# Performance work log

Measured on AMD Instinct MI355X. Metric: run time of the kernel, lower is better.

Reference implementation:

```python
import jax, jax.numpy as jnp
import numpy as np

N = 100000      # nodes
E = 1600000     # edges (avg degree 16)
F = 128         # feature dim (in == out)
H = 4           # heads
ALPHA = 0.2     # leaky relu slope


def setup_inputs() -> dict:
    key = jax.random.key(0)
    k1, k2, k3, k4, k5 = jax.random.split(key, 5)
    inputs = jax.random.normal(k1, (N, F), dtype=jnp.float32)
    # ensure every node appears as a destination row (src of message) so rowsum > 0
    src = jnp.concatenate([jnp.arange(N, dtype=jnp.int32),
                           jax.random.randint(k2, (E - N,), 0, N, dtype=jnp.int32)])
    dst = jax.random.randint(k3, (E,), 0, N, dtype=jnp.int32)
    edge = jnp.stack([src, dst])  # [2, E], rows = adj.indices()
    adj_values = jax.random.uniform(k4, (E,), dtype=jnp.float32)
    W = jnp.ones((H, F), dtype=jnp.float32)  # nn.init.ones_ per head
    stdv = 1.0 / np.sqrt(2.0 * F)
    a = jax.random.uniform(k5, (H, 2 * F), dtype=jnp.float32, minval=-stdv, maxval=stdv)
    return {"inputs": inputs, "edge": edge, "adj_values": adj_values, "W": W, "a": a}


def reference(inputs, edge, adj_values, W, a):
    src, dst = edge[0], edge[1]
    acc = jnp.zeros_like(inputs)
    for k in range(H):  # small fixed head loop (distinct params per head)
        h = inputs * W[k]                       # [N, F] elementwise scale
        # a.mm([h_src; h_dst]) decomposes into per-node partial scores
        s_src = h @ a[k, :F]                    # [N]
        s_dst = h @ a[k, F:]                    # [N]
        e = jnp.exp(jax.nn.leaky_relu(s_src[src] + s_dst[dst], ALPHA)) * adj_values  # [E]
        rowsum = jax.ops.segment_sum(e, src, num_segments=N)               # [N]
        h_prime = jax.ops.segment_sum(e[:, None] * h[dst], src, num_segments=N)  # [N, F]
        acc = acc + jax.nn.elu(h_prime / rowsum[:, None])  # concat=True -> elu
    return acc / H  # mean over heads
```

## Files before the change

kernel.cpp:

```cpp
#include <hip/hip_runtime.h>

#define FDIM   128
#define HEADS  4
#define ALPHA  0.2f
#define DMASK  0x03FFFFFF
#define PT     4096
#define NBMAX  1568

typedef float v2f __attribute__((ext_vector_type(2)));
typedef __attribute__((ext_vector_type(8))) short bf16x8;
typedef __attribute__((ext_vector_type(4))) float f32x4;
typedef __attribute__((ext_vector_type(4))) unsigned u32x4;

__global__ __launch_bounds__(256) void score_kernel(
    const float* __restrict__ x, const float* __restrict__ W,
    const float* __restrict__ a, float* __restrict__ s_src,
    float* __restrict__ s_dst, unsigned int* __restrict__ xb,
    const int* __restrict__ src, int* __restrict__ hist,
    int E, int HB, int n) {
  __shared__ int h[NBMAX];
  int lane = threadIdx.x & 63;
  int node = (blockIdx.x << 2) + (threadIdx.x >> 6);
  if (node < n) {
    const float2* x2 = (const float2*)x;
    const float2* W2 = (const float2*)W;
    const float2* a2 = (const float2*)a;
    float2 xv = x2[(size_t)node * 64 + lane];

    unsigned int u0 = __float_as_uint(xv.x);
    unsigned int u1 = __float_as_uint(xv.y);
    u0 += 0x7fffu + ((u0 >> 16) & 1u);
    u1 += 0x7fffu + ((u1 >> 16) & 1u);
    xb[(size_t)node * 64 + lane] = (u0 >> 16) | (u1 & 0xffff0000u);

    float p[8];
#pragma unroll
    for (int k = 0; k < HEADS; k++) {
      float2 wv = W2[k * 64 + lane];
      float hx = xv.x * wv.x, hy = xv.y * wv.y;
      float2 as_ = a2[k * 128 + lane];
      float2 ad_ = a2[k * 128 + 64 + lane];
      p[k]     = hx * as_.x + hy * as_.y;
      p[4 + k] = hx * ad_.x + hy * ad_.y;
    }

    bool h5 = (lane & 32) != 0;
    float q[4];
#pragma unroll
    for (int k = 0; k < 4; k++) {
      float send = h5 ? p[k] : p[4 + k];
      float got = __shfl_xor(send, 32);
      q[k] = (h5 ? p[4 + k] : p[k]) + got;
    }
    bool h4 = (lane & 16) != 0;
    float r[2];
#pragma unroll
    for (int j = 0; j < 2; j++) {
      float send = h4 ? q[j] : q[2 + j];
      float got = __shfl_xor(send, 16);
      r[j] = (h4 ? q[2 + j] : q[j]) + got;
    }
    bool h3 = (lane & 8) != 0;
    float send = h3 ? r[0] : r[1];
    float got = __shfl_xor(send, 8);
    float v = (h3 ? r[1] : r[0]) + got;
    v += __shfl_xor(v, 1);
    v += __shfl_xor(v, 2);
    v += __shfl_xor(v, 4);
    if ((lane & 7) == 0) {
      int s = lane >> 3;
      if (s < 4) s_src[node * HEADS + s] = v;
      else       s_dst[node * HEADS + (s - 4)] = v;
    }
  }

  int b = blockIdx.x;
  if (b < HB) {
    int t = threadIdx.x;
    int NB = (n + 63) >> 6;
    for (int i = t; i < NB; i += 256) h[i] = 0;
    __syncthreads();
    int base = b * 8192;
#pragma unroll 4
    for (int j = 0; j < 32; j++) {
      int i = base + j * 256 + t;
      if (i < E) atomicAdd(&h[src[i] >> 6], 1);
    }
    __syncthreads();
    for (int i = t; i < NB; i += 256)
      if (h[i]) atomicAdd(&hist[i], h[i]);
  }
}

__global__ __launch_bounds__(256) void scan_kernel(const int* __restrict__ hist,
                                                   int* __restrict__ fine_ptr,
                                                   int* __restrict__ cursor,
                                                   int NB, int E) {
  __shared__ int lds[256];
  int t = threadIdx.x;
  int loc[8];
  int s = 0;
#pragma unroll
  for (int j = 0; j < 8; j++) {
    int idx = t * 8 + j;
    loc[j] = (idx < NB) ? hist[idx] : 0;
    s += loc[j];
  }
  lds[t] = s;
  __syncthreads();
  for (int off = 1; off < 256; off <<= 1) {
    int xv = (t >= off) ? lds[t - off] : 0;
    __syncthreads();
    lds[t] += xv;
    __syncthreads();
  }
  int run = lds[t] - s;
#pragma unroll
  for (int j = 0; j < 8; j++) {
    int idx = t * 8 + j;
    if (idx < NB) {
      fine_ptr[idx] = run;
      cursor[idx]   = run;
    }
    run += loc[j];
  }
  if (t == 0) fine_ptr[NB] = E;
}

__global__ __launch_bounds__(256) void partition_kernel(
    const int* __restrict__ src, const int* __restrict__ dst,
    const float* __restrict__ adj, int* __restrict__ cursor,
    int2* __restrict__ ebuf, int E, int NB) {
  __shared__ int h[NBMAX];
  __shared__ int sc[NBMAX];
  __shared__ int bg[NBMAX];
  __shared__ unsigned short keyarr[PT];
  __shared__ int2 es[PT];
  __shared__ int lds[256];

  int t = threadIdx.x;
  int base = blockIdx.x * PT;
  for (int i = t; i < NB; i += 256) h[i] = 0;
  __syncthreads();

  int ssrc[16];
#pragma unroll
  for (int j = 0; j < 16; j++) {
    int i = base + j * 256 + t;
    ssrc[j] = (i < E) ? src[i] : -1;
    if (ssrc[j] >= 0) atomicAdd(&h[ssrc[j] >> 6], 1);
  }
  __syncthreads();

  int loc[8];
  int s = 0;
#pragma unroll
  for (int j = 0; j < 8; j++) {
    int idx = t * 8 + j;
    loc[j] = (idx < NB) ? h[idx] : 0;
    s += loc[j];
  }
  lds[t] = s;
  __syncthreads();
  for (int off = 1; off < 256; off <<= 1) {
    int xv = (t >= off) ? lds[t - off] : 0;
    __syncthreads();
    lds[t] += xv;
    __syncthreads();
  }
  int run = lds[t] - s;
#pragma unroll
  for (int j = 0; j < 8; j++) {
    int idx = t * 8 + j;
    if (idx < NB) sc[idx] = run;
    run += loc[j];
  }
  __syncthreads();

  for (int i = t; i < NB; i += 256)
    if (h[i]) bg[i] = atomicAdd(&cursor[i], h[i]);
  __syncthreads();

#pragma unroll
  for (int j = 0; j < 16; j++) {
    if (ssrc[j] >= 0) {
      int i = base + j * 256 + t;
      int k = ssrc[j] >> 6;
      int slot = atomicAdd(&sc[k], 1);
      int2 pk;
      pk.x = (int)(((unsigned)(ssrc[j] & 63) << 26) | (unsigned)dst[i]);
      pk.y = __float_as_int(adj[i]);
      es[slot] = pk;
      keyarr[slot] = (unsigned short)k;
    }
  }
  __syncthreads();

  int tc = E - base; if (tc > PT) tc = PT;
  for (int s2 = t; s2 < tc; s2 += 256) {
    int k = keyarr[s2];
    int rank = s2 - (sc[k] - h[k]);
    ebuf[bg[k] + rank] = es[s2];
  }
}

__global__ __launch_bounds__(256, 4) void aggregate_kernel(
    const unsigned int* __restrict__ xb, const float* __restrict__ W,
    const float* __restrict__ s_src, const float* __restrict__ s_dst,
    const int* __restrict__ fine_ptr, const int2* __restrict__ ebuf,
    float* __restrict__ out, int n) {
  __shared__ int2  es[512];
  __shared__ unsigned short xrow[4][32][130];
  __shared__ float evls[4][192];
  __shared__ int   nbeg[17];
  __shared__ int   nrun[16];
  __shared__ int   h[16];

  int t = threadIdx.x, bb = blockIdx.x;
  int b0 = bb >> 2, qtr = bb & 3;
  int lane = t & 63, wid = t >> 6;
  int beg = fine_ptr[b0];
  int L   = fine_ptr[b0 + 1] - beg;

  if (t < 16) h[t] = 0;
  __syncthreads();
  for (int i = t; i < L; i += 256) {
    int kk = (unsigned)ebuf[beg + i].x >> 26;
    if ((kk >> 4) == qtr) atomicAdd(&h[kk & 15], 1);
  }
  __syncthreads();
  if (t < 16) {
    int v = h[t];
#pragma unroll
    for (int off = 1; off < 16; off <<= 1) {
      int u = __shfl_up(v, off);
      if (lane >= off) v += u;
    }
    nbeg[t + 1] = v;
    nrun[t] = v - h[t];
    if (t == 0) nbeg[0] = 0;
  }
  __syncthreads();
  for (int i = t; i < L; i += 256) {
    int2 pk = ebuf[beg + i];
    int kk = (unsigned)pk.x >> 26;
    if ((kk >> 4) == qtr) {
      int slot = atomicAdd(&nrun[kk & 15], 1);
      es[slot] = pk;
    }
  }
  __syncthreads();

  int el = lane & 31;
  int hp = lane >> 5;
  int kb = (lane >> 4) << 3;
  int ha = lane & 3;
  int na = (lane & 15) >> 2;
  unsigned dsel = (lane & 1) ? 0x07060302u : 0x05040100u;

  bf16x8 bones;
#pragma unroll
  for (int j = 0; j < 8; j++) bones[j] = (short)0x3F80;

  f32x4 acc[8];
#pragma unroll
  for (int c = 0; c < 8; c++) acc[c] = (f32x4){0.f, 0.f, 0.f, 0.f};
  f32x4 accR = (f32x4){0.f, 0.f, 0.f, 0.f};

  int wbase = nbeg[wid * 4];
  int wend  = nbeg[wid * 4 + 4];
  int gb = (b0 << 6) + (qtr << 4) + wid * 4;

  for (int cb = wbase; cb < wend; cb += 32) {
    int rem = wend - cb;
    int2 pk{0, 0};
    if (el < rem) pk = es[cb + el];

    asm volatile("s_waitcnt lgkmcnt(0)" ::: "memory");
#pragma unroll
    for (int j = 0; j < 32; j++) {
      int dd = __builtin_amdgcn_readlane(pk.x, j) & DMASK;
      __builtin_amdgcn_global_load_lds(
          (const __attribute__((address_space(1))) unsigned int*)
              (xb + (((size_t)(unsigned)dd) << 6) + lane),
          (__attribute__((address_space(3))) unsigned int*)(&xrow[wid][j][0]),
          4, 0, 0);
    }

    unsigned kk = (unsigned)pk.x >> 26;
    int own_e = (int)(kk & 3);
    int dv = pk.x & DMASK;
    int ng = (b0 << 6) + (qtr << 4) + (int)(kk & 15);
    float2 sv  = *(const float2*)&s_src[ng * 4 + 2 * hp];
    float2 dvv = *(const float2*)&s_dst[dv * 4 + 2 * hp];
    float adjv = __int_as_float(pk.y);
    float s0 = sv.x + dvv.x; s0 = (s0 >= 0.f) ? s0 : ALPHA * s0;
    float s1 = sv.y + dvv.y; s1 = (s1 >= 0.f) ? s1 : ALPHA * s1;
    float e0 = __expf(s0) * adjv;
    float e1 = __expf(s1) * adjv;
    if (el >= rem) { e0 = 0.f; e1 = 0.f; }
    *(float2*)&evls[wid][el * 6 + 2 * hp] = float2{e0, e1};
    evls[wid][el * 6 + 4] = __int_as_float(own_e);

    unsigned hw0, hw1, hw2, hw3, lw0, lw1, lw2, lw3;
#define ABUILD(JP, HW, LW) {                                          \
      int k0 = kb + 2 * (JP), k1 = k0 + 1;                            \
      float m0 = evls[wid][k0 * 6 + ha];                              \
      float m1 = evls[wid][k1 * 6 + ha];                              \
      int o0 = __float_as_int(evls[wid][k0 * 6 + 4]);                 \
      int o1 = __float_as_int(evls[wid][k1 * 6 + 4]);                 \
      m0 = (o0 == na) ? m0 : 0.f;                                     \
      m1 = (o1 == na) ? m1 : 0.f;                                     \
      unsigned u0 = __float_as_uint(m0), u1 = __float_as_uint(m1);    \
      unsigned r0 = u0 + 0x7fffu + ((u0 >> 16) & 1u);                 \
      unsigned r1 = u1 + 0x7fffu + ((u1 >> 16) & 1u);                 \
      HW = __builtin_amdgcn_perm(r1, r0, 0x07060302u);                \
      float l0 = m0 - __uint_as_float(r0 & 0xffff0000u);              \
      float l1 = m1 - __uint_as_float(r1 & 0xffff0000u);              \
      LW = __builtin_amdgcn_perm(__float_as_uint(l1),                 \
                                 __float_as_uint(l0), 0x07060302u); }
    ABUILD(0, hw0, lw0)
    ABUILD(1, hw1, lw1)
    ABUILD(2, hw2, lw2)
    ABUILD(3, hw3, lw3)
#undef ABUILD
    bf16x8 ahi = __builtin_bit_cast(bf16x8, (u32x4){hw0, hw1, hw2, hw3});
    bf16x8 alo = __builtin_bit_cast(bf16x8, (u32x4){lw0, lw1, lw2, lw3});

    asm volatile("s_waitcnt vmcnt(0)" ::: "memory");
    int fb = lane & 14;
#pragma unroll
    for (int cc = 0; cc < 8; cc++) {
      unsigned dw[8];
#pragma unroll
      for (int j = 0; j < 8; j++)
        dw[j] = *(const unsigned*)&xrow[wid][kb + j][cc * 16 + fb];
      u32x4 bw = { __builtin_amdgcn_perm(dw[1], dw[0], dsel),
                   __builtin_amdgcn_perm(dw[3], dw[2], dsel),
                   __builtin_amdgcn_perm(dw[5], dw[4], dsel),
                   __builtin_amdgcn_perm(dw[7], dw[6], dsel) };
      bf16x8 bfrag = __builtin_bit_cast(bf16x8, bw);
      acc[cc] = __builtin_amdgcn_mfma_f32_16x16x32_bf16(ahi, bfrag, acc[cc], 0, 0, 0);
      acc[cc] = __builtin_amdgcn_mfma_f32_16x16x32_bf16(alo, bfrag, acc[cc], 0, 0, 0);
    }
    accR = __builtin_amdgcn_mfma_f32_16x16x32_bf16(ahi, bones, accR, 0, 0, 0);
    accR = __builtin_amdgcn_mfma_f32_16x16x32_bf16(alo, bones, accR, 0, 0, 0);
  }

  float rinv0 = __builtin_amdgcn_rcpf(accR[0]);
  float rinv1 = __builtin_amdgcn_rcpf(accR[1]);
  float rinv2 = __builtin_amdgcn_rcpf(accR[2]);
  float rinv3 = __builtin_amdgcn_rcpf(accR[3]);
  int ng4 = gb + (lane >> 4);
  bool valid = ng4 < n;
  int fl = lane & 15;
#pragma unroll
  for (int cc = 0; cc < 8; cc++) {
    int f = cc * 16 + fl;
    float o = 0.f;
    float v0 = acc[cc][0] * W[0 * 128 + f] * rinv0;
    o += (v0 > 0.f) ? v0 : (__expf(v0) - 1.f);
    float v1 = acc[cc][1] * W[1 * 128 + f] * rinv1;
    o += (v1 > 0.f) ? v1 : (__expf(v1) - 1.f);
    float v2 = acc[cc][2] * W[2 * 128 + f] * rinv2;
    o += (v2 > 0.f) ? v2 : (__expf(v2) - 1.f);
    float v3 = acc[cc][3] * W[3 * 128 + f] * rinv3;
    o += (v3 > 0.f) ? v3 : (__expf(v3) - 1.f);
    if (valid) out[(size_t)ng4 * 128 + f] = o * 0.25f;
  }
}

extern "C" void kernel_launch(void* const* d_in, const int* in_sizes, int n_in,
                              void* d_out, int out_size, void* d_ws, size_t ws_size,
                              hipStream_t stream) {
  const float* x   = (const float*)d_in[0];
  const int*   edg = (const int*)d_in[1];
  const float* adj = (const float*)d_in[2];
  const float* W   = (const float*)d_in[3];
  const float* a   = (const float*)d_in[4];
  float* out = (float*)d_out;

  int E = in_sizes[2];
  int n = in_sizes[0] / FDIM;
  const int* src = edg;
  const int* dst = edg + E;
  int NB = (n + 63) >> 6;
  int HB = (E + 8191) / 8192;

  auto align = [](size_t v) { return (v + 255) & ~(size_t)255; };
  char* ws = (char*)d_ws;
  int*   fine_ptr = (int*)ws;          ws += align((size_t)(NB + 1) * 4);
  int*   cursor   = (int*)ws;          ws += align((size_t)NB * 4);
  int*   hist     = (int*)ws;          ws += align((size_t)NB * 4);
  int2*  ebuf     = (int2*)ws;         ws += align((size_t)E * 8);
  float* s_src    = (float*)ws;        ws += align((size_t)n * HEADS * 4);
  float* s_dst    = (float*)ws;        ws += align((size_t)n * HEADS * 4);
  unsigned int* xb = (unsigned int*)ws; ws += align((size_t)n * 64 * 4);

  hipMemsetAsync(hist, 0, (size_t)NB * 4, stream);

  score_kernel<<<(n + 3) / 4, 256, 0, stream>>>(x, W, a, s_src, s_dst, xb,
                                                src, hist, E, HB, n);
  scan_kernel<<<1, 256, 0, stream>>>(hist, fine_ptr, cursor, NB, E);
  partition_kernel<<<(E + PT - 1) / PT, 256, 0, stream>>>(src, dst, adj, cursor,
                                                          ebuf, E, NB);
  aggregate_kernel<<<NB * 4, 256, 0, stream>>>(xb, W, s_src, s_dst, fine_ptr,
                                               ebuf, out, n);
}
```

Baseline: 287.5 us.

## Process whole 64-node bucket per block with register double-buffered gathers

The aggregate kernel now launches one block per 64-node bucket instead of four quarter-blocks. Each wave walks its 16 nodes in groups of four, and the edge bucket is read and histogrammed once per block rather than four times. Direct global-to-LDS gathers are replaced by register loads into two buffers, so the next 32-edge window is fetched while the current window is scored, staged to LDS and fed through MFMA. This removes the redundant bucket scans and hides gather latency. The cost is more registers (two 32-entry row buffers, launch bounds lowered to 3), a larger shared edge array sized for at most 2048 edges per bucket, and four times fewer blocks.

```diff
diff --git a/kernel.cpp b/kernel.cpp
--- a/kernel.cpp
+++ b/kernel.cpp
@@ -7,7 +7,6 @@
 #define PT     4096
 #define NBMAX  1568
 
-typedef float v2f __attribute__((ext_vector_type(2)));
 typedef __attribute__((ext_vector_type(8))) short bf16x8;
 typedef __attribute__((ext_vector_type(4))) float f32x4;
 typedef __attribute__((ext_vector_type(4))) unsigned u32x4;
@@ -204,35 +203,32 @@
   }
 }
 
-__global__ __launch_bounds__(256, 4) void aggregate_kernel(
+__global__ __launch_bounds__(256, 3) void aggregate_kernel(
     const unsigned int* __restrict__ xb, const float* __restrict__ W,
     const float* __restrict__ s_src, const float* __restrict__ s_dst,
     const int* __restrict__ fine_ptr, const int2* __restrict__ ebuf,
     float* __restrict__ out, int n) {
-  __shared__ int2  es[512];
+  __shared__ int2  es[2048];
   __shared__ unsigned short xrow[4][32][130];
   __shared__ float evls[4][192];
-  __shared__ int   nbeg[17];
-  __shared__ int   nrun[16];
-  __shared__ int   h[16];
-
-  int t = threadIdx.x, bb = blockIdx.x;
-  int b0 = bb >> 2, qtr = bb & 3;
+  __shared__ int   nbeg[65];
+  __shared__ int   nrun[64];
+  __shared__ int   h[64];
+
+  int t = threadIdx.x, b = blockIdx.x;
   int lane = t & 63, wid = t >> 6;
-  int beg = fine_ptr[b0];
-  int L   = fine_ptr[b0 + 1] - beg;
-
-  if (t < 16) h[t] = 0;
-  __syncthreads();
-  for (int i = t; i < L; i += 256) {
-    int kk = (unsigned)ebuf[beg + i].x >> 26;
-    if ((kk >> 4) == qtr) atomicAdd(&h[kk & 15], 1);
-  }
-  __syncthreads();
-  if (t < 16) {
+  int beg = fine_ptr[b];
+  int L   = fine_ptr[b + 1] - beg;
+
+  if (t < 64) h[t] = 0;
+  __syncthreads();
+  for (int i = t; i < L; i += 256)
+    atomicAdd(&h[(unsigned)ebuf[beg + i].x >> 26], 1);
+  __syncthreads();
+  if (t < 64) {
     int v = h[t];
 #pragma unroll
-    for (int off = 1; off < 16; off <<= 1) {
+    for (int off = 1; off < 64; off <<= 1) {
       int u = __shfl_up(v, off);
       if (lane >= off) v += u;
     }
@@ -244,10 +240,8 @@
   for (int i = t; i < L; i += 256) {
     int2 pk = ebuf[beg + i];
     int kk = (unsigned)pk.x >> 26;
-    if ((kk >> 4) == qtr) {
-      int slot = atomicAdd(&nrun[kk & 15], 1);
-      es[slot] = pk;
-    }
+    int slot = atomicAdd(&nrun[kk], 1);
+    es[slot] = pk;
   }
   __syncthreads();
 
@@ -267,32 +261,33 @@
   for (int c = 0; c < 8; c++) acc[c] = (f32x4){0.f, 0.f, 0.f, 0.f};
   f32x4 accR = (f32x4){0.f, 0.f, 0.f, 0.f};
 
-  int wbase = nbeg[wid * 4];
-  int wend  = nbeg[wid * 4 + 4];
-  int gb = (b0 << 6) + (qtr << 4) + wid * 4;
-
-  for (int cb = wbase; cb < wend; cb += 32) {
-    int rem = wend - cb;
+  int nb0 = wid * 16;
+
+  auto issue_win = [&](int qw, int sw, int2& pko, float2& dvo, float2& svo,
+                       unsigned (&rw)[32]) {
+    int endq = nbeg[nb0 + qw * 4 + 4];
+    int rem = endq - sw;
     int2 pk{0, 0};
-    if (el < rem) pk = es[cb + el];
-
-    asm volatile("s_waitcnt lgkmcnt(0)" ::: "memory");
+    if (el < rem) pk = es[sw + el];
+    pko = pk;
+    unsigned kk = (unsigned)pk.x >> 26;
+    int dv = pk.x & DMASK;
+    int ng = (b << 6) + (int)kk;
+    svo = *(const float2*)&s_src[ng * 4 + 2 * hp];
+    dvo = *(const float2*)&s_dst[dv * 4 + 2 * hp];
 #pragma unroll
     for (int j = 0; j < 32; j++) {
       int dd = __builtin_amdgcn_readlane(pk.x, j) & DMASK;
-      __builtin_amdgcn_global_load_lds(
-          (const __attribute__((address_space(1))) unsigned int*)
-              (xb + (((size_t)(unsigned)dd) << 6) + lane),
-          (__attribute__((address_space(3))) unsigned int*)(&xrow[wid][j][0]),
-          4, 0, 0);
-    }
-
+      rw[j] = xb[(((size_t)(unsigned)dd) << 6) + lane];
+    }
+  };
+
+  auto compute_win = [&](int qw, int sw, int2 pk, float2 dvv, float2 sv,
+                         unsigned (&rw)[32]) {
+    int endq = nbeg[nb0 + qw * 4 + 4];
+    int rem = endq - sw;
     unsigned kk = (unsigned)pk.x >> 26;
     int own_e = (int)(kk & 3);
-    int dv = pk.x & DMASK;
-    int ng = (b0 << 6) + (qtr << 4) + (int)(kk & 15);
-    float2 sv  = *(const float2*)&s_src[ng * 4 + 2 * hp];
-    float2 dvv = *(const float2*)&s_dst[dv * 4 + 2 * hp];
     float adjv = __int_as_float(pk.y);
     float s0 = sv.x + dvv.x; s0 = (s0 >= 0.f) ? s0 : ALPHA * s0;
     float s1 = sv.y + dvv.y; s1 = (s1 >= 0.f) ? s1 : ALPHA * s1;
@@ -301,6 +296,10 @@
     if (el >= rem) { e0 = 0.f; e1 = 0.f; }
     *(float2*)&evls[wid][el * 6 + 2 * hp] = float2{e0, e1};
     evls[wid][el * 6 + 4] = __int_as_float(own_e);
+
+#pragma unroll
+    for (int j = 0; j < 32; j++)
+      *(unsigned*)&xrow[wid][j][2 * lane] = rw[j];
 
     unsigned hw0, hw1, hw2, hw3, lw0, lw1, lw2, lw3;
 #define ABUILD(JP, HW, LW) {                                          \
@@ -327,7 +326,6 @@
     bf16x8 ahi = __builtin_bit_cast(bf16x8, (u32x4){hw0, hw1, hw2, hw3});
     bf16x8 alo = __builtin_bit_cast(bf16x8, (u32x4){lw0, lw1, lw2, lw3});
 
-    asm volatile("s_waitcnt vmcnt(0)" ::: "memory");
     int fb = lane & 14;
 #pragma unroll
     for (int cc = 0; cc < 8; cc++) {
@@ -345,28 +343,60 @@
     }
     accR = __builtin_amdgcn_mfma_f32_16x16x32_bf16(ahi, bones, accR, 0, 0, 0);
     accR = __builtin_amdgcn_mfma_f32_16x16x32_bf16(alo, bones, accR, 0, 0, 0);
-  }
-
-  float rinv0 = __builtin_amdgcn_rcpf(accR[0]);
-  float rinv1 = __builtin_amdgcn_rcpf(accR[1]);
-  float rinv2 = __builtin_amdgcn_rcpf(accR[2]);
-  float rinv3 = __builtin_amdgcn_rcpf(accR[3]);
-  int ng4 = gb + (lane >> 4);
-  bool valid = ng4 < n;
-  int fl = lane & 15;
-#pragma unroll
-  for (int cc = 0; cc < 8; cc++) {
-    int f = cc * 16 + fl;
-    float o = 0.f;
-    float v0 = acc[cc][0] * W[0 * 128 + f] * rinv0;
-    o += (v0 > 0.f) ? v0 : (__expf(v0) - 1.f);
-    float v1 = acc[cc][1] * W[1 * 128 + f] * rinv1;
-    o += (v1 > 0.f) ? v1 : (__expf(v1) - 1.f);
-    float v2 = acc[cc][2] * W[2 * 128 + f] * rinv2;
-    o += (v2 > 0.f) ? v2 : (__expf(v2) - 1.f);
-    float v3 = acc[cc][3] * W[3 * 128 + f] * rinv3;
-    o += (v3 > 0.f) ? v3 : (__expf(v3) - 1.f);
-    if (valid) out[(size_t)ng4 * 128 + f] = o * 0.25f;
+  };
+
+  auto epilogue = [&](int q) {
+    float rinv0 = __builtin_amdgcn_rcpf(accR[0]);
+    float rinv1 = __builtin_amdgcn_rcpf(accR[1]);
+    float rinv2 = __builtin_amdgcn_rcpf(accR[2]);
+    float rinv3 = __builtin_amdgcn_rcpf(accR[3]);
+    int ng4 = (b << 6) + nb0 + q * 4 + (lane >> 4);
+    bool valid = ng4 < n;
+    int fl = lane & 15;
+#pragma unroll
+    for (int cc = 0; cc < 8; cc++) {
+      int f = cc * 16 + fl;
+      float o = 0.f;
+      float v0 = acc[cc][0] * W[0 * 128 + f] * rinv0;
+      o += (v0 > 0.f) ? v0 : (__expf(v0) - 1.f);
+      float v1 = acc[cc][1] * W[1 * 128 + f] * rinv1;
+      o += (v1 > 0.f) ? v1 : (__expf(v1) - 1.f);
+      float v2 = acc[cc][2] * W[2 * 128 + f] * rinv2;
+      o += (v2 > 0.f) ? v2 : (__expf(v2) - 1.f);
+      float v3 = acc[cc][3] * W[3 * 128 + f] * rinv3;
+      o += (v3 > 0.f) ? v3 : (__expf(v3) - 1.f);
+      if (valid) out[(size_t)ng4 * 128 + f] = o * 0.25f;
+    }
+#pragma unroll
+    for (int c = 0; c < 8; c++) acc[c] = (f32x4){0.f, 0.f, 0.f, 0.f};
+    accR = (f32x4){0.f, 0.f, 0.f, 0.f};
+  };
+
+  int2 pkA, pkB; float2 dvA, dvB, svA, svB;
+  unsigned rwA[32], rwB[32];
+
+  int qc = 0, sc = nbeg[nb0];
+  while (qc < 4 && sc >= nbeg[nb0 + qc * 4 + 4]) {
+    qc++;
+    if (qc < 4) sc = nbeg[nb0 + qc * 4];
+  }
+  if (qc < 4) issue_win(qc, sc, pkA, dvA, svA, rwA);
+  bool curA = true;
+  while (qc < 4) {
+    int qn = qc, sn = sc + 32;
+    while (qn < 4 && sn >= nbeg[nb0 + qn * 4 + 4]) {
+      qn++;
+      if (qn < 4) sn = nbeg[nb0 + qn * 4];
+    }
+    if (curA) {
+      if (qn < 4) issue_win(qn, sn, pkB, dvB, svB, rwB);
+      compute_win(qc, sc, pkA, dvA, svA, rwA);
+    } else {
+      if (qn < 4) issue_win(qn, sn, pkA, dvA, svA, rwA);
+      compute_win(qc, sc, pkB, dvB, svB, rwB);
+    }
+    if (qn != qc) epilogue(qc);
+    qc = qn; sc = sn; curA = !curA;
   }
 }
 
@@ -404,6 +434,6 @@
   scan_kernel<<<1, 256, 0, stream>>>(hist, fine_ptr, cursor, NB, E);
   partition_kernel<<<(E + PT - 1) / PT, 256, 0, stream>>>(src, dst, adj, cursor,
                                                           ebuf, E, NB);
-  aggregate_kernel<<<NB * 4, 256, 0, stream>>>(xb, W, s_src, s_dst, fine_ptr,
-                                               ebuf, out, n);
+  aggregate_kernel<<<NB, 256, 0, stream>>>(xb, W, s_src, s_dst, fine_ptr,
+                                           ebuf, out, n);
 }
```

After: 581.5 us. 2.02x slower.
